# Optimization experiments

Measured on AMD Instinct MI355X. Metric: run time of the kernel, lower is better.

The kernel has to match this reference:

```python
import jax, jax.numpy as jnp
import numpy as np

N = 50000      # nodes
E = 800000     # edges (avg degree 16)
D = 64         # num_node_features
H = 64         # hidden_channels
G = 512        # graphs in batch
OUT = 32       # final linear output
NEG_SLOPE = 0.2


def setup_inputs() -> dict:
    key = jax.random.key(0)
    ks = jax.random.split(key, 20)
    s = 0.1  # param init scale
    inp = {
        "x": jax.random.normal(ks[0], (N, D), jnp.float32),
        "edge_index": jax.random.randint(ks[1], (2, E), 0, N, dtype=jnp.int64),
        "batch": jnp.sort(jax.random.randint(ks[2], (N,), 0, G, dtype=jnp.int64)),
        # GATv2 layer 1 (D -> H)
        "Wl1": jax.random.normal(ks[3], (D, H), jnp.float32) * s,
        "bl1": jnp.zeros((H,), jnp.float32),
        "Wr1": jax.random.normal(ks[4], (D, H), jnp.float32) * s,
        "br1": jnp.zeros((H,), jnp.float32),
        "att1": jax.random.normal(ks[5], (H,), jnp.float32) * s,
        "bias1": jnp.zeros((H,), jnp.float32),
        # GATv2 layer 2 (H -> H)
        "Wl2": jax.random.normal(ks[6], (H, H), jnp.float32) * s,
        "bl2": jnp.zeros((H,), jnp.float32),
        "Wr2": jax.random.normal(ks[7], (H, H), jnp.float32) * s,
        "br2": jnp.zeros((H,), jnp.float32),
        "att2": jax.random.normal(ks[8], (H,), jnp.float32) * s,
        "bias2": jnp.zeros((H,), jnp.float32),
        # final classifier
        "lin_w": jax.random.normal(ks[9], (H, OUT), jnp.float32) * s,
        "lin_b": jnp.zeros((OUT,), jnp.float32),
    }
    return inp


def _gatv2(x, src, dst, Wl, bl, Wr, br, att, bias):
    # GATv2Conv, heads=1, PyG semantics: messages flow src -> dst
    xl = x @ Wl + bl                       # [N, H] source transform (also the message)
    xr = x @ Wr + br                       # [N, H] destination transform
    z = xl[src] + xr[dst]                  # [E, H] gather
    e = jax.nn.leaky_relu(z, NEG_SLOPE) @ att  # [E] edge scores
    # segment softmax over edges grouped by destination node
    m = jax.ops.segment_max(e, dst, num_segments=N)   # [N]
    ex = jnp.exp(e - m[dst])                          # [E]
    denom = jax.ops.segment_sum(ex, dst, num_segments=N)  # [N]
    alpha = ex / denom[dst]                            # [E]
    out = jax.ops.segment_sum(alpha[:, None] * xl[src], dst, num_segments=N)  # [N, H]
    return out + bias


def reference(x, edge_index, batch,
              Wl1, bl1, Wr1, br1, att1, bias1,
              Wl2, bl2, Wr2, br2, att2, bias2,
              lin_w, lin_b):
    src, dst = edge_index[0], edge_index[1]
    h = jax.nn.relu(_gatv2(x, src, dst, Wl1, bl1, Wr1, br1, att1, bias1))
    h = jax.nn.relu(_gatv2(h, src, dst, Wl2, bl2, Wr2, br2, att2, bias2))
    # global mean pool over graphs
    sums = jax.ops.segment_sum(h, batch, num_segments=G)          # [G, H]
    cnts = jax.ops.segment_sum(jnp.ones((h.shape[0],), h.dtype), batch, num_segments=G)
    pooled = sums / jnp.maximum(cnts, 1.0)[:, None]
    # dropout(p=0.5) is identity at inference
    return pooled @ lin_w + lin_b                                  # [G, 32]
```

## Files before the change

kernel.cpp:

```cpp
#include <hip/hip_runtime.h>
#include <hip/hip_fp16.h>
#include <math.h>


#define ELLC    48
#define OVF_CAP 65536
#define ECHUNK  2048

typedef int      vint4 __attribute__((ext_vector_type(4)));
typedef _Float16 half4 __attribute__((ext_vector_type(4)));

#define GROWS 32
__device__ __forceinline__ void dual_gemm_slim(
    int bid, int t,
    const float* __restrict__ X,
    const float* __restrict__ Wl, const float* __restrict__ bl,
    const float* __restrict__ Wr, const float* __restrict__ br,
    _Float16* __restrict__ xl, float* __restrict__ xr, int n,
    float* xS) {
    int row0 = bid * GROWS;
    for (int i = t; i < GROWS * 16; i += 256) {
        int r = row0 + (i >> 4);
        float4 v = make_float4(0.f, 0.f, 0.f, 0.f);
        if (r < n) v = ((const float4*)(X + (size_t)r * 64))[i & 15];
        ((float4*)xS)[i] = v;
    }
    __syncthreads();
    int h  = t & 63;
    int rb = t >> 6;
    float accl[8], accr[8];
#pragma unroll
    for (int i = 0; i < 8; ++i) { accl[i] = 0.f; accr[i] = 0.f; }
#pragma unroll 4
    for (int d = 0; d < 64; ++d) {
        float wl = Wl[d * 64 + h];
        float wr = Wr[d * 64 + h];
#pragma unroll
        for (int i = 0; i < 8; ++i) {
            float xv = xS[(rb + 4 * i) * 64 + d];
            accl[i] += xv * wl;
            accr[i] += xv * wr;
        }
    }
    float blv = bl[h], brv = br[h];
#pragma unroll
    for (int i = 0; i < 8; ++i) {
        int r = row0 + rb + 4 * i;
        if (r < n) {
            xl[(size_t)r * 64 + h] = (_Float16)(accl[i] + blv);
            xr[(size_t)r * 64 + h] = accr[i] + brv;
        }
    }
}

__global__ __launch_bounds__(256) void dual_gemm64_kernel(
    const float* __restrict__ X,
    const float* __restrict__ Wl, const float* __restrict__ bl,
    const float* __restrict__ Wr, const float* __restrict__ br,
    _Float16* __restrict__ xl, float* __restrict__ xr, int n) {
    __shared__ float xS[GROWS * 64];
    dual_gemm_slim(blockIdx.x, threadIdx.x, X, Wl, bl, Wr, br, xl, xr, n, xS);
}

__global__ __launch_bounds__(256) void fill_gemm_kernel(
    const int* __restrict__ src, const int* __restrict__ dst,
    int* __restrict__ cnt, unsigned short* __restrict__ ell,
    int* __restrict__ novf, int* __restrict__ ovf_dst, int* __restrict__ ovf_src,
    int E, int N, int psize, int fb, int ggrid,
    const float* __restrict__ X,
    const float* __restrict__ Wl, const float* __restrict__ bl,
    const float* __restrict__ Wr, const float* __restrict__ br,
    _Float16* __restrict__ xl, float* __restrict__ xr) {
    __shared__ float xS[GROWS * 64];
    int b = blockIdx.x;
    int q = b / 24, r = b % 24;
    if (r >= 16) {
        int vg = q * 8 + (r - 16);
        if (vg < ggrid)
            dual_gemm_slim(vg, threadIdx.x, X, Wl, bl, Wr, br, xl, xr, N, xS);
        return;
    }
    int vb = q * 16 + r;
    if (vb >= fb) return;
    int t     = threadIdx.x;
    int chunk = vb >> 3;
    int p     = vb & 7;
    int d0    = p * psize;
    int d1    = min(N, d0 + psize);
    int e0    = chunk * ECHUNK;
    int e1    = min(E, e0 + ECHUNK);
    int nq    = (e1 - e0) >> 2;
    const vint4* dst4 = (const vint4*)(dst + e0);
    const vint4* src4 = (const vint4*)(src + e0);

    auto scatter4 = [&](vint4 dv, vint4 sv) {
#pragma unroll
        for (int k = 0; k < 4; ++k) {
            int d = dv[k];
            int s = sv[k];
            if (d >= d0 && d < d1) {
                int pos = atomicAdd(&cnt[d], 1);
                if (pos < ELLC) {
                    ell[d * ELLC + pos] = (unsigned short)s;
                } else {
                    int j = atomicAdd(novf, 1);
                    if (j < OVF_CAP) { ovf_dst[j] = d; ovf_src[j] = s; }
                }
            }
        }
    };

    if (nq == (ECHUNK >> 2)) {
        vint4 dvA = __builtin_nontemporal_load(&dst4[t]);
        vint4 svA = __builtin_nontemporal_load(&src4[t]);
        vint4 dvB = __builtin_nontemporal_load(&dst4[t + 256]);
        vint4 svB = __builtin_nontemporal_load(&src4[t + 256]);
        scatter4(dvA, svA);
        scatter4(dvB, svB);
    } else {
        for (int qq = t; qq < nq; qq += 256) {
            vint4 dv = __builtin_nontemporal_load(&dst4[qq]);
            vint4 sv = __builtin_nontemporal_load(&src4[qq]);
            scatter4(dv, sv);
        }
        for (int e = e0 + (nq << 2) + t; e < e1; e += 256) {
            int d = dst[e];
            if (d >= d0 && d < d1) {
                int pos = atomicAdd(&cnt[d], 1);
                int s   = src[e];
                if (pos < ELLC) {
                    ell[d * ELLC + pos] = (unsigned short)s;
                } else {
                    int j = atomicAdd(novf, 1);
                    if (j < OVF_CAP) { ovf_dst[j] = d; ovf_src[j] = s; }
                }
            }
        }
    }
}

__global__ __launch_bounds__(256) void gat_aggregate_kernel(
    const _Float16* __restrict__ xl, const float* __restrict__ xr,
    const int* __restrict__ cnt, const unsigned short* __restrict__ ell,
    const int* __restrict__ novf, const int* __restrict__ ovf_dst,
    const int* __restrict__ ovf_src,
    const float* __restrict__ att, const float* __restrict__ bias,
    float* __restrict__ out, int n) {
    int wid  = (blockIdx.x * blockDim.x + threadIdx.x) >> 6;
    int lane = threadIdx.x & 63;
    if (wid >= n) return;
    int g = lane >> 4;
    int l = lane & 15;
    int d = wid;

    float4 att4 = ((const float4*)att)[l];
    float4 b4   = ((const float4*)bias)[l];
    int deg_d = cnt[d];
    int nd  = min(deg_d, ELLC);
    int beg = d * ELLC;

    if (deg_d == 0) {
        if (g == 0) {
            float4 v;
            v.x = fmaxf(b4.x, 0.f); v.y = fmaxf(b4.y, 0.f);
            v.z = fmaxf(b4.z, 0.f); v.w = fmaxf(b4.w, 0.f);
            ((float4*)(out + (size_t)d * 64))[l] = v;
        }
        return;
    }

    int myidx = 0;
    if (lane < ELLC) myidx = (int)ell[beg + lane];
    int i_first = __shfl(myidx, 0);

    float4 xr4 = ((const float4*)(xr + (size_t)d * 64))[l];
    float  s   = 0.f;
    float4 acc = make_float4(0.f, 0.f, 0.f, 0.f);

#pragma unroll 6
    for (int k = 0; k * 8 < nd; ++k) {
        int  sa = k * 8 + g, sb = sa + 4;
        bool aa = sa < nd,   ab = sb < nd;
        int  i0 = __shfl(myidx, sa); if (!aa) i0 = i_first;
        int  i1 = __shfl(myidx, sb); if (!ab) i1 = i_first;
        half4 h0 = ((const half4*)(xl + (size_t)i0 * 64))[l];
        half4 h1 = ((const half4*)(xl + (size_t)i1 * 64))[l];
        float4 x0 = make_float4((float)h0[0], (float)h0[1], (float)h0[2], (float)h0[3]);
        float4 x1 = make_float4((float)h1[0], (float)h1[1], (float)h1[2], (float)h1[3]);
        float z, c0 = 0.f, c1 = 0.f;
        z = x0.x + xr4.x; c0 += ((z > 0.f) ? z : 0.2f * z) * att4.x;
        z = x0.y + xr4.y; c0 += ((z > 0.f) ? z : 0.2f * z) * att4.y;
        z = x0.z + xr4.z; c0 += ((z > 0.f) ? z : 0.2f * z) * att4.z;
        z = x0.w + xr4.w; c0 += ((z > 0.f) ? z : 0.2f * z) * att4.w;
        z = x1.x + xr4.x; c1 += ((z > 0.f) ? z : 0.2f * z) * att4.x;
        z = x1.y + xr4.y; c1 += ((z > 0.f) ? z : 0.2f * z) * att4.y;
        z = x1.z + xr4.z; c1 += ((z > 0.f) ? z : 0.2f * z) * att4.z;
        z = x1.w + xr4.w; c1 += ((z > 0.f) ? z : 0.2f * z) * att4.w;
#pragma unroll
        for (int sh = 8; sh >= 1; sh >>= 1) {
            c0 += __shfl_xor(c0, sh);
            c1 += __shfl_xor(c1, sh);
        }
        float w0 = aa ? __expf(fminf(c0, 30.f)) : 0.f;
        float w1 = ab ? __expf(fminf(c1, 30.f)) : 0.f;
        s += w0 + w1;
        acc.x += w0 * x0.x + w1 * x1.x;
        acc.y += w0 * x0.y + w1 * x1.y;
        acc.z += w0 * x0.z + w1 * x1.z;
        acc.w += w0 * x0.w + w1 * x1.w;
    }
    if (deg_d > ELLC) {
        int no = min(*novf, OVF_CAP);
        for (int j = g; j < no; j += 4) {
            bool active = (ovf_dst[j] == d);
            int  i0     = active ? ovf_src[j] : i_first;
            half4 h0 = ((const half4*)(xl + (size_t)i0 * 64))[l];
            float4 x0 = make_float4((float)h0[0], (float)h0[1], (float)h0[2], (float)h0[3]);
            float z, c0 = 0.f;
            z = x0.x + xr4.x; c0 += ((z > 0.f) ? z : 0.2f * z) * att4.x;
            z = x0.y + xr4.y; c0 += ((z > 0.f) ? z : 0.2f * z) * att4.y;
            z = x0.z + xr4.z; c0 += ((z > 0.f) ? z : 0.2f * z) * att4.z;
            z = x0.w + xr4.w; c0 += ((z > 0.f) ? z : 0.2f * z) * att4.w;
#pragma unroll
            for (int sh = 8; sh >= 1; sh >>= 1) c0 += __shfl_xor(c0, sh);
            float w0 = active ? __expf(fminf(c0, 30.f)) : 0.f;
            s += w0;
            acc.x += w0 * x0.x;
            acc.y += w0 * x0.y;
            acc.z += w0 * x0.z;
            acc.w += w0 * x0.w;
        }
    }
#pragma unroll
    for (int mask = 16; mask <= 32; mask <<= 1) {
        s     += __shfl_xor(s, mask);
        acc.x += __shfl_xor(acc.x, mask);
        acc.y += __shfl_xor(acc.y, mask);
        acc.z += __shfl_xor(acc.z, mask);
        acc.w += __shfl_xor(acc.w, mask);
    }
    if (g == 0) {
        float inv = (s > 0.f) ? (1.f / s) : 0.f;
        float4 v;
        v.x = fmaxf(acc.x * inv + b4.x, 0.f);
        v.y = fmaxf(acc.y * inv + b4.y, 0.f);
        v.z = fmaxf(acc.z * inv + b4.z, 0.f);
        v.w = fmaxf(acc.w * inv + b4.w, 0.f);
        ((float4*)(out + (size_t)d * 64))[l] = v;
    }
}

__global__ __launch_bounds__(256) void pool_kernel(
    const float* __restrict__ h, const int* __restrict__ batch,
    float* __restrict__ sums, float* __restrict__ cnts, int n, int nwaves) {
    int wid  = (blockIdx.x * blockDim.x + threadIdx.x) >> 6;
    int lane = threadIdx.x & 63;
    int per   = (n + nwaves - 1) / nwaves;
    int start = wid * per;
    int end   = min(n, start + per);
    if (start >= end) return;
    int cur   = batch[start];
    float acc = 0.f, cnt = 0.f;
    for (int i = start; i < end; ++i) {
        int g = batch[i];
        if (g != cur) {
            atomicAdd(&sums[cur * 64 + lane], acc);
            if (lane == 0) atomicAdd(&cnts[cur], cnt);
            acc = 0.f; cnt = 0.f; cur = g;
        }
        acc += h[(size_t)i * 64 + lane];
        cnt += 1.f;
    }
    atomicAdd(&sums[cur * 64 + lane], acc);
    if (lane == 0) atomicAdd(&cnts[cur], cnt);
}

__global__ __launch_bounds__(256) void final_kernel(
    const float* __restrict__ sums, const float* __restrict__ cnts,
    const float* __restrict__ lin_w, const float* __restrict__ lin_b,
    float* __restrict__ out, int total) {
    int tid = blockIdx.x * blockDim.x + threadIdx.x;
    if (tid >= total) return;
    int g = tid >> 5, o = tid & 31;
    float inv = 1.f / fmaxf(cnts[g], 1.f);
    float a = 0.f;
    for (int h = 0; h < 64; ++h) a += sums[g * 64 + h] * lin_w[h * 32 + o];
    out[tid] = a * inv + lin_b[o];
}

extern "C" void kernel_launch(void* const* d_in, const int* in_sizes, int n_in,
                              void* d_out, int out_size, void* d_ws, size_t ws_size,
                              hipStream_t stream) {
    const float* x     = (const float*)d_in[0];
    const int*   ei    = (const int*)d_in[1];
    const int*   batch = (const int*)d_in[2];
    const float* Wl1   = (const float*)d_in[3];
    const float* bl1   = (const float*)d_in[4];
    const float* Wr1   = (const float*)d_in[5];
    const float* br1   = (const float*)d_in[6];
    const float* att1  = (const float*)d_in[7];
    const float* bias1 = (const float*)d_in[8];
    const float* Wl2   = (const float*)d_in[9];
    const float* bl2   = (const float*)d_in[10];
    const float* Wr2   = (const float*)d_in[11];
    const float* br2   = (const float*)d_in[12];
    const float* att2  = (const float*)d_in[13];
    const float* bias2 = (const float*)d_in[14];
    const float* lin_w = (const float*)d_in[15];
    const float* lin_b = (const float*)d_in[16];
    float* out = (float*)d_out;

    const int N = in_sizes[0] / 64;
    const int E = in_sizes[1] / 2;
    const int G = out_size / 32;
    const int* src = ei;
    const int* dst = ei + E;

    char*  ws  = (char*)d_ws;
    size_t off = 0;
    auto alloc = [&](size_t bytes) -> void* {
        void* p = ws + off;
        off += bytes;
        off = (off + 255) & ~(size_t)255;
        return p;
    };
    _Float16* xl   = (_Float16*)alloc((size_t)N * 64 * sizeof(_Float16));
    float* xr      = (float*)alloc((size_t)N * 64 * sizeof(float));
    float* h1      = (float*)alloc((size_t)N * 64 * sizeof(float));
    int*   cnt     = (int*)alloc((size_t)N * sizeof(int));
    int*   novf    = (int*)alloc(256);
    float* sums    = (float*)alloc((size_t)G * 64 * sizeof(float));
    float* cnts    = (float*)alloc((size_t)G * sizeof(float));
    char*  zend    = ws + off;
    unsigned short* ell = (unsigned short*)alloc((size_t)N * ELLC * sizeof(unsigned short));
    int*   ovf_dst = (int*)alloc((size_t)OVF_CAP * sizeof(int));
    int*   ovf_src = (int*)alloc((size_t)OVF_CAP * sizeof(int));

    (void)hipMemsetAsync(cnt, 0, (size_t)(zend - (char*)cnt), stream);

    int ggrid  = (N + GROWS - 1) / GROWS;
    int agrid  = (N + 3) / 4;
    int nchunk = (E + ECHUNK - 1) / ECHUNK;
    int fb     = nchunk * 8;
    int psize  = (N + 7) / 8;
    int ngroups = max((fb + 15) / 16, (ggrid + 7) / 8);
    int igrid   = ngroups * 24;

    fill_gemm_kernel<<<igrid, 256, 0, stream>>>(
        src, dst, cnt, ell, novf, ovf_dst, ovf_src, E, N, psize, fb, ggrid,
        x, Wl1, bl1, Wr1, br1, xl, xr);

    gat_aggregate_kernel<<<agrid, 256, 0, stream>>>(
        xl, xr, cnt, ell, novf, ovf_dst, ovf_src, att1, bias1, h1, N);

    dual_gemm64_kernel<<<ggrid, 256, 0, stream>>>(h1, Wl2, bl2, Wr2, br2, xl, xr, N);
    gat_aggregate_kernel<<<agrid, 256, 0, stream>>>(
        xl, xr, cnt, ell, novf, ovf_dst, ovf_src, att2, bias2, h1, N);

    const int NWAVES = 2048;
    pool_kernel<<<512, 256, 0, stream>>>(h1, batch, sums, cnts, N, NWAVES);
    int total = G * 32;
    final_kernel<<<(total + 255) / 256, 256, 0, stream>>>(sums, cnts, lin_w, lin_b, out, total);
}
```

Baseline: 246.4 us.

## Store layer-1 output in fp16 and fuse mean-pooling into layer-2 aggregation

New measurement: 346.1 us. +40.5%, slower.

```diff
diff --git a/kernel.cpp b/kernel.cpp
--- a/kernel.cpp
+++ b/kernel.cpp
@@ -11,9 +11,10 @@
 typedef _Float16 half4 __attribute__((ext_vector_type(4)));
 
 #define GROWS 32
+template <typename T>
 __device__ __forceinline__ void dual_gemm_slim(
     int bid, int t,
-    const float* __restrict__ X,
+    const T* __restrict__ X,
     const float* __restrict__ Wl, const float* __restrict__ bl,
     const float* __restrict__ Wr, const float* __restrict__ br,
     _Float16* __restrict__ xl, float* __restrict__ xr, int n,
@@ -22,7 +23,14 @@
     for (int i = t; i < GROWS * 16; i += 256) {
         int r = row0 + (i >> 4);
         float4 v = make_float4(0.f, 0.f, 0.f, 0.f);
-        if (r < n) v = ((const float4*)(X + (size_t)r * 64))[i & 15];
+        if (r < n) {
+            if constexpr (sizeof(T) == 2) {
+                half4 hv = ((const half4*)(X + (size_t)r * 64))[i & 15];
+                v = make_float4((float)hv[0], (float)hv[1], (float)hv[2], (float)hv[3]);
+            } else {
+                v = ((const float4*)(X + (size_t)r * 64))[i & 15];
+            }
+        }
         ((float4*)xS)[i] = v;
     }
     __syncthreads();
@@ -53,13 +61,14 @@
     }
 }
 
-__global__ __launch_bounds__(256) void dual_gemm64_kernel(
-    const float* __restrict__ X,
+__global__ __launch_bounds__(256) void dual_gemm64_f16_kernel(
+    const _Float16* __restrict__ X,
     const float* __restrict__ Wl, const float* __restrict__ bl,
     const float* __restrict__ Wr, const float* __restrict__ br,
     _Float16* __restrict__ xl, float* __restrict__ xr, int n) {
     __shared__ float xS[GROWS * 64];
-    dual_gemm_slim(blockIdx.x, threadIdx.x, X, Wl, bl, Wr, br, xl, xr, n, xS);
+    dual_gemm_slim<_Float16>(blockIdx.x, threadIdx.x, X, Wl, bl, Wr, br,
+                             xl, xr, n, xS);
 }
 
 __global__ __launch_bounds__(256) void fill_gemm_kernel(
@@ -77,7 +86,8 @@
     if (r >= 16) {
         int vg = q * 8 + (r - 16);
         if (vg < ggrid)
-            dual_gemm_slim(vg, threadIdx.x, X, Wl, bl, Wr, br, xl, xr, N, xS);
+            dual_gemm_slim<float>(vg, threadIdx.x, X, Wl, bl, Wr, br,
+                                  xl, xr, N, xS);
         return;
     }
     int vb = q * 16 + r;
@@ -145,7 +155,9 @@
     const int* __restrict__ novf, const int* __restrict__ ovf_dst,
     const int* __restrict__ ovf_src,
     const float* __restrict__ att, const float* __restrict__ bias,
-    float* __restrict__ out, int n) {
+    _Float16* __restrict__ out16,
+    float* __restrict__ sums, float* __restrict__ cnts,
+    const int* __restrict__ batch, int n) {
     int wid  = (blockIdx.x * blockDim.x + threadIdx.x) >> 6;
     int lane = threadIdx.x & 63;
     if (wid >= n) return;
@@ -159,85 +171,78 @@
     int nd  = min(deg_d, ELLC);
     int beg = d * ELLC;
 
-    if (deg_d == 0) {
-        if (g == 0) {
-            float4 v;
-            v.x = fmaxf(b4.x, 0.f); v.y = fmaxf(b4.y, 0.f);
-            v.z = fmaxf(b4.z, 0.f); v.w = fmaxf(b4.w, 0.f);
-            ((float4*)(out + (size_t)d * 64))[l] = v;
-        }
-        return;
-    }
-
-    int myidx = 0;
-    if (lane < ELLC) myidx = (int)ell[beg + lane];
-    int i_first = __shfl(myidx, 0);
-
-    float4 xr4 = ((const float4*)(xr + (size_t)d * 64))[l];
     float  s   = 0.f;
     float4 acc = make_float4(0.f, 0.f, 0.f, 0.f);
 
+    if (deg_d > 0) {
+        int myidx = 0;
+        if (lane < ELLC) myidx = (int)ell[beg + lane];
+        int i_first = __shfl(myidx, 0);
+
+        float4 xr4 = ((const float4*)(xr + (size_t)d * 64))[l];
+
 #pragma unroll 6
-    for (int k = 0; k * 8 < nd; ++k) {
-        int  sa = k * 8 + g, sb = sa + 4;
-        bool aa = sa < nd,   ab = sb < nd;
-        int  i0 = __shfl(myidx, sa); if (!aa) i0 = i_first;
-        int  i1 = __shfl(myidx, sb); if (!ab) i1 = i_first;
-        half4 h0 = ((const half4*)(xl + (size_t)i0 * 64))[l];
-        half4 h1 = ((const half4*)(xl + (size_t)i1 * 64))[l];
-        float4 x0 = make_float4((float)h0[0], (float)h0[1], (float)h0[2], (float)h0[3]);
-        float4 x1 = make_float4((float)h1[0], (float)h1[1], (float)h1[2], (float)h1[3]);
-        float z, c0 = 0.f, c1 = 0.f;
-        z = x0.x + xr4.x; c0 += ((z > 0.f) ? z : 0.2f * z) * att4.x;
-        z = x0.y + xr4.y; c0 += ((z > 0.f) ? z : 0.2f * z) * att4.y;
-        z = x0.z + xr4.z; c0 += ((z > 0.f) ? z : 0.2f * z) * att4.z;
-        z = x0.w + xr4.w; c0 += ((z > 0.f) ? z : 0.2f * z) * att4.w;
-        z = x1.x + xr4.x; c1 += ((z > 0.f) ? z : 0.2f * z) * att4.x;
-        z = x1.y + xr4.y; c1 += ((z > 0.f) ? z : 0.2f * z) * att4.y;
-        z = x1.z + xr4.z; c1 += ((z > 0.f) ? z : 0.2f * z) * att4.z;
-        z = x1.w + xr4.w; c1 += ((z > 0.f) ? z : 0.2f * z) * att4.w;
-#pragma unroll
-        for (int sh = 8; sh >= 1; sh >>= 1) {
-            c0 += __shfl_xor(c0, sh);
-            c1 += __shfl_xor(c1, sh);
-        }
-        float w0 = aa ? __expf(fminf(c0, 30.f)) : 0.f;
-        float w1 = ab ? __expf(fminf(c1, 30.f)) : 0.f;
-        s += w0 + w1;
-        acc.x += w0 * x0.x + w1 * x1.x;
-        acc.y += w0 * x0.y + w1 * x1.y;
-        acc.z += w0 * x0.z + w1 * x1.z;
-        acc.w += w0 * x0.w + w1 * x1.w;
-    }
-    if (deg_d > ELLC) {
-        int no = min(*novf, OVF_CAP);
-        for (int j = g; j < no; j += 4) {
-            bool active = (ovf_dst[j] == d);
-            int  i0     = active ? ovf_src[j] : i_first;
+        for (int k = 0; k * 8 < nd; ++k) {
+            int  sa = k * 8 + g, sb = sa + 4;
+            bool aa = sa < nd,   ab = sb < nd;
+            int  i0 = __shfl(myidx, sa); if (!aa) i0 = i_first;
+            int  i1 = __shfl(myidx, sb); if (!ab) i1 = i_first;
             half4 h0 = ((const half4*)(xl + (size_t)i0 * 64))[l];
+            half4 h1 = ((const half4*)(xl + (size_t)i1 * 64))[l];
             float4 x0 = make_float4((float)h0[0], (float)h0[1], (float)h0[2], (float)h0[3]);
-            float z, c0 = 0.f;
+            float4 x1 = make_float4((float)h1[0], (float)h1[1], (float)h1[2], (float)h1[3]);
+            float z, c0 = 0.f, c1 = 0.f;
             z = x0.x + xr4.x; c0 += ((z > 0.f) ? z : 0.2f * z) * att4.x;
             z = x0.y + xr4.y; c0 += ((z > 0.f) ? z : 0.2f * z) * att4.y;
             z = x0.z + xr4.z; c0 += ((z > 0.f) ? z : 0.2f * z) * att4.z;
             z = x0.w + xr4.w; c0 += ((z > 0.f) ? z : 0.2f * z) * att4.w;
-#pragma unroll
-            for (int sh = 8; sh >= 1; sh >>= 1) c0 += __shfl_xor(c0, sh);
-            float w0 = active ? __expf(fminf(c0, 30.f)) : 0.f;
-            s += w0;
-            acc.x += w0 * x0.x;
-            acc.y += w0 * x0.y;
-            acc.z += w0 * x0.z;
-            acc.w += w0 * x0.w;
-        }
-    }
-#pragma unroll
-    for (int mask = 16; mask <= 32; mask <<= 1) {
-        s     += __shfl_xor(s, mask);
-        acc.x += __shfl_xor(acc.x, mask);
-        acc.y += __shfl_xor(acc.y, mask);
-        acc.z += __shfl_xor(acc.z, mask);
-        acc.w += __shfl_xor(acc.w, mask);
+            z = x1.x + xr4.x; c1 += ((z > 0.f) ? z : 0.2f * z) * att4.x;
+            z = x1.y + xr4.y; c1 += ((z > 0.f) ? z : 0.2f * z) * att4.y;
+            z = x1.z + xr4.z; c1 += ((z > 0.f) ? z : 0.2f * z) * att4.z;
+            z = x1.w + xr4.w; c1 += ((z > 0.f) ? z : 0.2f * z) * att4.w;
+#pragma unroll
+            for (int sh = 8; sh >= 1; sh >>= 1) {
+                c0 += __shfl_xor(c0, sh);
+                c1 += __shfl_xor(c1, sh);
+            }
+            float w0 = aa ? __expf(fminf(c0, 30.f)) : 0.f;
+            float w1 = ab ? __expf(fminf(c1, 30.f)) : 0.f;
+            s += w0 + w1;
+            acc.x += w0 * x0.x + w1 * x1.x;
+            acc.y += w0 * x0.y + w1 * x1.y;
+            acc.z += w0 * x0.z + w1 * x1.z;
+            acc.w += w0 * x0.w + w1 * x1.w;
+        }
+        if (deg_d > ELLC) {
+            int no = min(*novf, OVF_CAP);
+            for (int j = g; j < no; j += 4) {
+                bool active = (ovf_dst[j] == d);
+                int  i0     = active ? ovf_src[j] : i_first;
+                half4 h0 = ((const half4*)(xl + (size_t)i0 * 64))[l];
+                float4 x0 = make_float4((float)h0[0], (float)h0[1], (float)h0[2], (float)h0[3]);
+                float z, c0 = 0.f;
+                z = x0.x + xr4.x; c0 += ((z > 0.f) ? z : 0.2f * z) * att4.x;
+                z = x0.y + xr4.y; c0 += ((z > 0.f) ? z : 0.2f * z) * att4.y;
+                z = x0.z + xr4.z; c0 += ((z > 0.f) ? z : 0.2f * z) * att4.z;
+                z = x0.w + xr4.w; c0 += ((z > 0.f) ? z : 0.2f * z) * att4.w;
+#pragma unroll
+                for (int sh = 8; sh >= 1; sh >>= 1) c0 += __shfl_xor(c0, sh);
+                float w0 = active ? __expf(fminf(c0, 30.f)) : 0.f;
+                s += w0;
+                acc.x += w0 * x0.x;
+                acc.y += w0 * x0.y;
+                acc.z += w0 * x0.z;
+                acc.w += w0 * x0.w;
+            }
+        }
+#pragma unroll
+        for (int mask = 16; mask <= 32; mask <<= 1) {
+            s     += __shfl_xor(s, mask);
+            acc.x += __shfl_xor(acc.x, mask);
+            acc.y += __shfl_xor(acc.y, mask);
+            acc.z += __shfl_xor(acc.z, mask);
+            acc.w += __shfl_xor(acc.w, mask);
+        }
     }
     if (g == 0) {
         float inv = (s > 0.f) ? (1.f / s) : 0.f;
@@ -246,33 +251,21 @@
         v.y = fmaxf(acc.y * inv + b4.y, 0.f);
         v.z = fmaxf(acc.z * inv + b4.z, 0.f);
         v.w = fmaxf(acc.w * inv + b4.w, 0.f);
-        ((float4*)(out + (size_t)d * 64))[l] = v;
-    }
-}
-
-__global__ __launch_bounds__(256) void pool_kernel(
-    const float* __restrict__ h, const int* __restrict__ batch,
-    float* __restrict__ sums, float* __restrict__ cnts, int n, int nwaves) {
-    int wid  = (blockIdx.x * blockDim.x + threadIdx.x) >> 6;
-    int lane = threadIdx.x & 63;
-    int per   = (n + nwaves - 1) / nwaves;
-    int start = wid * per;
-    int end   = min(n, start + per);
-    if (start >= end) return;
-    int cur   = batch[start];
-    float acc = 0.f, cnt = 0.f;
-    for (int i = start; i < end; ++i) {
-        int g = batch[i];
-        if (g != cur) {
-            atomicAdd(&sums[cur * 64 + lane], acc);
-            if (lane == 0) atomicAdd(&cnts[cur], cnt);
-            acc = 0.f; cnt = 0.f; cur = g;
-        }
-        acc += h[(size_t)i * 64 + lane];
-        cnt += 1.f;
-    }
-    atomicAdd(&sums[cur * 64 + lane], acc);
-    if (lane == 0) atomicAdd(&cnts[cur], cnt);
+        if (out16) {
+            half4 hv;
+            hv[0] = (_Float16)v.x; hv[1] = (_Float16)v.y;
+            hv[2] = (_Float16)v.z; hv[3] = (_Float16)v.w;
+            ((half4*)(out16 + (size_t)d * 64))[l] = hv;
+        } else {
+            int grp = batch[d];
+            float* sp = sums + (size_t)grp * 64 + 4 * l;
+            atomicAdd(sp + 0, v.x);
+            atomicAdd(sp + 1, v.y);
+            atomicAdd(sp + 2, v.z);
+            atomicAdd(sp + 3, v.w);
+            if (l == 0) atomicAdd(&cnts[grp], 1.f);
+        }
+    }
 }
 
 __global__ __launch_bounds__(256) void final_kernel(
@@ -326,7 +319,7 @@
     };
     _Float16* xl   = (_Float16*)alloc((size_t)N * 64 * sizeof(_Float16));
     float* xr      = (float*)alloc((size_t)N * 64 * sizeof(float));
-    float* h1      = (float*)alloc((size_t)N * 64 * sizeof(float));
+    _Float16* h1   = (_Float16*)alloc((size_t)N * 64 * sizeof(_Float16));
     int*   cnt     = (int*)alloc((size_t)N * sizeof(int));
     int*   novf    = (int*)alloc(256);
     float* sums    = (float*)alloc((size_t)G * 64 * sizeof(float));
@@ -351,14 +344,16 @@
         x, Wl1, bl1, Wr1, br1, xl, xr);
 
     gat_aggregate_kernel<<<agrid, 256, 0, stream>>>(
-        xl, xr, cnt, ell, novf, ovf_dst, ovf_src, att1, bias1, h1, N);
-
-    dual_gemm64_kernel<<<ggrid, 256, 0, stream>>>(h1, Wl2, bl2, Wr2, br2, xl, xr, N);
+        xl, xr, cnt, ell, novf, ovf_dst, ovf_src, att1, bias1,
+        h1, nullptr, nullptr, nullptr, N);
+
+    dual_gemm64_f16_kernel<<<ggrid, 256, 0, stream>>>(
+        h1, Wl2, bl2, Wr2, br2, xl, xr, N);
+
     gat_aggregate_kernel<<<agrid, 256, 0, stream>>>(
-        xl, xr, cnt, ell, novf, ovf_dst, ovf_src, att2, bias2, h1, N);
-
-    const int NWAVES = 2048;
-    pool_kernel<<<512, 256, 0, stream>>>(h1, batch, sums, cnts, N, NWAVES);
+        xl, xr, cnt, ell, novf, ovf_dst, ovf_src, att2, bias2,
+        nullptr, sums, cnts, batch, N);
+
     int total = G * 32;
     final_kernel<<<(total + 255) / 256, 256, 0, stream>>>(sums, cnts, lin_w, lin_b, out, total);
 }
```
